# Performance work log

Hardware: AMD Instinct MI355X
Metric: run time of the kernel (lower is better)

Reference implementation:

```python
import jax, jax.numpy as jnp
import numpy as np
import math

BETA = 0.25      # CONFIG['vq_commitment_beta']
DECAY = 0.99     # CONFIG['vq_decay']
EPS = 1e-5

N, D, K = 262144, 64, 512


def setup_inputs() -> dict:
    key = jax.random.key(0)
    k1, k2, k3, k4 = jax.random.split(key, 4)
    z_real = jax.random.normal(k1, (N, D), jnp.float32)
    z_imag = jax.random.normal(k2, (N, D), jnp.float32)
    # embedding init: uniform(-1/K, 1/K); ema_w initialized as a clone
    emb_w = jax.random.uniform(k3, (K, 2 * D), jnp.float32, -1.0 / K, 1.0 / K)
    ema_cluster_size = jnp.zeros((K,), jnp.float32)
    ema_w = emb_w
    return {
        "z_real": z_real,
        "z_imag": z_imag,
        "emb_w": emb_w,
        "ema_cluster_size": ema_cluster_size,
        "ema_w": ema_w,
    }


def reference(z_real, z_imag, emb_w, ema_cluster_size, ema_w):
    n, d = z_real.shape
    k = emb_w.shape[0]
    z_flat = jnp.concatenate([z_real, z_imag], axis=-1)          # [N, 2D]
    # squared euclidean distances to codebook rows
    x_sq = jnp.sum(z_flat ** 2, axis=1, keepdims=True)           # [N, 1]
    y_sq = jnp.sum(emb_w ** 2, axis=1)                           # [K]
    dist = x_sq + y_sq - 2.0 * (z_flat @ emb_w.T)                # [N, K]
    indices = jnp.argmin(dist, axis=-1)                          # [N] int
    z_q = emb_w[indices]                                         # [N, 2D]

    # training-mode EMA update (one-hot matmuls expressed as segment sums)
    ones = jnp.ones((n,), z_flat.dtype)
    n_total = jax.ops.segment_sum(ones, indices, num_segments=k)        # [K]
    new_cluster = ema_cluster_size * DECAY + (1.0 - DECAY) * n_total
    tot = new_cluster.sum()
    cluster_size = (new_cluster + EPS) / (tot + k * EPS) * tot
    dw = jax.ops.segment_sum(z_flat, indices, num_segments=k)           # [K, 2D]
    new_ema_w = ema_w * DECAY + (1.0 - DECAY) * dw
    new_emb_w = new_ema_w / cluster_size[:, None]

    # commitment loss per sample (z_q detached)
    loss_sample = BETA * jnp.mean((jax.lax.stop_gradient(z_q) - z_flat) ** 2, axis=-1)
    # straight-through estimator
    z_q_st = z_flat + jax.lax.stop_gradient(z_q - z_flat)

    probs = n_total / n
    norm_entropy = -jnp.sum(probs * jnp.log(probs + 1e-10)) / math.log(k)

    zq_real = z_q_st[:, :d]
    zq_imag = z_q_st[:, d:]
    return (zq_real, zq_imag, loss_sample, indices, norm_entropy,
            new_emb_w, new_cluster, new_ema_w)
```

## Files before the change

kernel.cpp:

```cpp
#include <hip/hip_runtime.h>

#define NROWS 262144
#define DD 64
#define D2 128
#define KK 512

#define O_ZQR 0
#define O_ZQI 16777216
#define O_LOSS 33554432
#define O_IDX 33816576
#define O_ENT 34078720
#define O_EMB 34078721
#define O_NCL 34144257
#define O_EMA 34144769

typedef __bf16 bf16x8 __attribute__((ext_vector_type(8)));
typedef float f32x4 __attribute__((ext_vector_type(4)));

__device__ __forceinline__ float comb8(const float r[8]) {
  return __fadd_rn(__fadd_rn(__fadd_rn(r[0], r[1]), __fadd_rn(r[2], r[3])),
                   __fadd_rn(__fadd_rn(r[4], r[5]), __fadd_rn(r[6], r[7])));
}

__device__ __forceinline__ ushort f2bf(float x) {
  union { float f; unsigned u; } a; a.f = x;
  unsigned r = (a.u + 0x7FFFu + ((a.u >> 16) & 1u)) >> 16;
  return (ushort)r;
}

__global__ __launch_bounds__(256) void prep_kernel(const float* __restrict__ emb,
    float* __restrict__ ysq, int* __restrict__ nt, float* __restrict__ dw) {
  int t = blockIdx.x * 256 + threadIdx.x;
  dw[t] = 0.f;
  if (t < KK) {
    nt[t] = 0;
    const float* a = emb + t * D2;
    float r[8];
#pragma unroll
    for (int q = 0; q < 8; ++q) { float v = a[q]; r[q] = __fmul_rn(v, v); }
    for (int m = 1; m < 16; ++m)
#pragma unroll
      for (int q = 0; q < 8; ++q) { float v = a[8 * m + q]; r[q] = __fadd_rn(r[q], __fmul_rn(v, v)); }
    ysq[t] = comb8(r);
  }
}

#define BMR 128
#define DELTA 1e-3f
#define LCAP 2048

__global__ __launch_bounds__(512, 2) void vq_mfma(
    const float* __restrict__ zr, const float* __restrict__ zi,
    const float* __restrict__ emb, const float* __restrict__ ysq,
    float* __restrict__ out_zqr, float* __restrict__ out_zqi,
    float* __restrict__ out_loss, float* __restrict__ out_idx,
    int* __restrict__ nt) {
  __shared__ __align__(16) float zf[BMR * 132];
  __shared__ __align__(16) ushort Ab[BMR * 136];
  __shared__ __align__(16) ushort Bb[128 * 136];
  __shared__ float ysql[KK];
  __shared__ float xsql[BMR];
  __shared__ float rowmin[BMR];
  __shared__ ushort lst[LCAP];
  __shared__ float rD[LCAP];
  __shared__ int cnt;
  __shared__ int idxr[BMR];

  const int tid = threadIdx.x;
  const int rowBase = blockIdx.x * BMR;
  const int wv = tid >> 6;
  const int lane = tid & 63;

#pragma unroll
  for (int r = 0; r < 8; ++r) {
    int fidx = r * 512 + tid;
    int row = fidx >> 5, g = fidx & 31;
    float4 v;
    if (g < 16) v = *(const float4*)(zr + (size_t)(rowBase + row) * DD + g * 4);
    else        v = *(const float4*)(zi + (size_t)(rowBase + row) * DD + (g - 16) * 4);
    *(float4*)&zf[row * 132 + g * 4] = v;
  }
  ysql[tid] = ysq[tid];
  if (tid == 0) cnt = 0;
  __syncthreads();

  if (tid < BMR) {
    const float* zp = zf + tid * 132;
    float r8[8];
#pragma unroll
    for (int q = 0; q < 8; ++q) { float z = zp[q]; r8[q] = __fmul_rn(z, z); }
    for (int m = 1; m < 16; ++m)
#pragma unroll
      for (int q = 0; q < 8; ++q) { float z = zp[8 * m + q]; r8[q] = __fadd_rn(r8[q], __fmul_rn(z, z)); }
    xsql[tid] = comb8(r8);
  }
  for (int l = tid; l < BMR * 32; l += 512) {
    int row = l >> 5, seg = l & 31;
    const float* zp = &zf[row * 132 + seg * 4];
    ushort4 u;
    u.x = f2bf(zp[0]); u.y = f2bf(zp[1]); u.z = f2bf(zp[2]); u.w = f2bf(zp[3]);
    *(ushort4*)&Ab[row * 136 + seg * 4] = u;
  }
  __syncthreads();

  bf16x8 af[4];
#pragma unroll
  for (int t = 0; t < 4; ++t)
    af[t] = *(const bf16x8*)&Ab[(16 * wv + (lane & 15)) * 136 + t * 32 + (lane >> 4) * 8];

  float m4[4] = {3.4e38f, 3.4e38f, 3.4e38f, 3.4e38f};

#pragma unroll 1
  for (int phase = 0; phase < 2; ++phase) {
#pragma unroll 1
    for (int c = 0; c < 4; ++c) {
      __syncthreads();
      for (int l = tid; l < 128 * 32; l += 512) {
        int code = l >> 5, seg = l & 31;
        float4 v = *(const float4*)(emb + (size_t)(c * 128 + code) * D2 + seg * 4);
        ushort4 u;
        u.x = f2bf(v.x); u.y = f2bf(v.y); u.z = f2bf(v.z); u.w = f2bf(v.w);
        *(ushort4*)&Bb[code * 136 + seg * 4] = u;
      }
      __syncthreads();

      f32x4 acc[8];
#pragma unroll
      for (int j = 0; j < 8; ++j) acc[j] = (f32x4){0.f, 0.f, 0.f, 0.f};
#pragma unroll
      for (int j = 0; j < 8; ++j)
#pragma unroll
        for (int t = 0; t < 4; ++t) {
          bf16x8 bv = *(const bf16x8*)&Bb[(j * 16 + (lane & 15)) * 136 + t * 32 + (lane >> 4) * 8];
          acc[j] = __builtin_amdgcn_mfma_f32_16x16x32_bf16(af[t], bv, acc[j], 0, 0, 0);
        }

      if (phase == 0) {
#pragma unroll
        for (int j = 0; j < 8; ++j) {
          float y = ysql[c * 128 + j * 16 + (lane & 15)];
#pragma unroll
          for (int r = 0; r < 4; ++r)
            m4[r] = fminf(m4[r], fmaf(-2.f, acc[j][r], y));
        }
      } else {
#pragma unroll
        for (int j = 0; j < 8; ++j) {
          int code = c * 128 + j * 16 + (lane & 15);
          float y = ysql[code];
#pragma unroll
          for (int r = 0; r < 4; ++r) {
            float s = fmaf(-2.f, acc[j][r], y);
            int row = 16 * wv + (lane >> 4) * 4 + r;
            if (s <= rowmin[row] + DELTA) {
              int e = atomicAdd(&cnt, 1);
              if (e < LCAP) lst[e] = (ushort)((row << 9) | code);
            }
          }
        }
      }
    }
    if (phase == 0) {
#pragma unroll
      for (int r = 0; r < 4; ++r) {
        m4[r] = fminf(m4[r], __shfl_xor(m4[r], 1, 64));
        m4[r] = fminf(m4[r], __shfl_xor(m4[r], 2, 64));
        m4[r] = fminf(m4[r], __shfl_xor(m4[r], 4, 64));
        m4[r] = fminf(m4[r], __shfl_xor(m4[r], 8, 64));
      }
      if ((lane & 15) == 0) {
#pragma unroll
        for (int r = 0; r < 4; ++r) rowmin[16 * wv + (lane >> 4) * 4 + r] = m4[r];
      }
      __syncthreads();
    }
  }
  __syncthreads();

  int n = cnt; if (n > LCAP) n = LCAP;
  for (int e = tid; e < n; e += 512) {
    int rc = lst[e];
    int row = rc >> 9, code = rc & 511;
    const float* wrow = emb + (size_t)code * D2;
    const float* zrow = zf + row * 132;
    float a = 0.f;
#pragma unroll 32
    for (int d = 0; d < D2; ++d) a = fmaf(zrow[d], wrow[d], a);
    rD[e] = fmaf(-2.f, a, __fadd_rn(xsql[row], ysql[code]));
  }
  __syncthreads();

  if (tid < BMR) {
    float bD = 3.4e38f; int bc = 1024;
    for (int e = 0; e < n; ++e) {
      int rc = lst[e];
      if ((rc >> 9) == tid) {
        float Dv = rD[e]; int cc = rc & 511;
        if (Dv < bD || (Dv == bD && cc < bc)) { bD = Dv; bc = cc; }
      }
    }
    idxr[tid] = bc;
    out_idx[rowBase + tid] = (float)bc;
    atomicAdd(&nt[bc], 1);
  }
  __syncthreads();

  {
    int m = tid & 15, rsub = tid >> 4;
#pragma unroll
    for (int p = 0; p < 8; ++p) {
      int half = p & 1;
      int row = (p >> 1) * 32 + rsub;
      int bi = idxr[row];
      float4 e4 = *(const float4*)(emb + (size_t)bi * D2 + half * DD + m * 4);
      float4 z4 = *(const float4*)&zf[row * 132 + half * DD + m * 4];
      float4 o;
      o.x = __fadd_rn(z4.x, __fsub_rn(e4.x, z4.x));
      o.y = __fadd_rn(z4.y, __fsub_rn(e4.y, z4.y));
      o.z = __fadd_rn(z4.z, __fsub_rn(e4.z, z4.z));
      o.w = __fadd_rn(z4.w, __fsub_rn(e4.w, z4.w));
      float* outp = half ? (out_zqi + (size_t)(rowBase + row) * DD + m * 4)
                         : (out_zqr + (size_t)(rowBase + row) * DD + m * 4);
      *(float4*)outp = o;
    }
  }

  if (tid < BMR) {
    int bi = idxr[tid];
    const float* erow = emb + (size_t)bi * D2;
    const float* zp = zf + tid * 132;
    float r8[8];
#pragma unroll
    for (int q = 0; q < 8; ++q) {
      float df = __fsub_rn(erow[q], zp[q]);
      r8[q] = __fmul_rn(df, df);
    }
    for (int m = 1; m < 16; ++m)
#pragma unroll
      for (int q = 0; q < 8; ++q) {
        float df = __fsub_rn(erow[8 * m + q], zp[8 * m + q]);
        r8[q] = __fadd_rn(r8[q], __fmul_rn(df, df));
      }
    float S = comb8(r8);
    out_loss[rowBase + tid] = __fmul_rn(0.25f, S / 128.0f);
  }
}

__global__ __launch_bounds__(256) void dw_scatter(const float* __restrict__ zr,
    const float* __restrict__ zi, const float* __restrict__ idxf,
    float* __restrict__ dw) {
  __shared__ float tab[KK * 32];
  int tid = threadIdx.x;
  int dc = blockIdx.x & 3;
  int rb = blockIdx.x >> 2;
  for (int l = tid; l < KK * 32; l += 256) tab[l] = 0.f;
  __syncthreads();
  int r = tid >> 5, c = tid & 31;
  const float* zsrc = (dc < 2) ? zr : zi;
  int colBase = (dc & 1) * 32;
  int rowBase = rb * 1024;
  int row = rowBase + r;
  int idx = (int)idxf[row];
  float v = zsrc[(size_t)row * DD + colBase + c];
  for (int it = 0; it < 127; ++it) {
    int nrow = rowBase + (it + 1) * 8 + r;
    int nidx = (int)idxf[nrow];
    float nv = zsrc[(size_t)nrow * DD + colBase + c];
    atomicAdd(&tab[idx * 32 + c], v);
    idx = nidx; v = nv;
  }
  atomicAdd(&tab[idx * 32 + c], v);
  __syncthreads();
  for (int l = tid; l < KK * 32; l += 256) {
    int k = l >> 5, cc = l & 31;
    atomicAdd(&dw[k * D2 + dc * 32 + cc], tab[l]);
  }
}

__device__ float pw128(const float* a) {
  float r[8];
#pragma unroll
  for (int q = 0; q < 8; ++q) r[q] = a[q];
  for (int m = 1; m < 16; ++m)
#pragma unroll
    for (int q = 0; q < 8; ++q) r[q] = __fadd_rn(r[q], a[8 * m + q]);
  return comb8(r);
}

__global__ __launch_bounds__(512) void finalize_kernel(const int* __restrict__ nt,
    const float* __restrict__ ema_cs, float* __restrict__ out_ncl,
    float* __restrict__ out_ent, float* __restrict__ csize) {
  __shared__ float arr[KK];
  __shared__ float term[KK];
  __shared__ float tot_s;
  int t = threadIdx.x;
  float c = (float)nt[t];
  float newc = __fadd_rn(__fmul_rn(ema_cs[t], 0.99f), __fmul_rn(0.01f, c));
  out_ncl[t] = newc;
  arr[t] = newc;
  float p = c / 262144.f;
  term[t] = __fmul_rn(p, logf(__fadd_rn(p, 1e-10f)));
  __syncthreads();
  if (t == 0) {
    float tot = __fadd_rn(__fadd_rn(pw128(arr), pw128(arr + 128)),
                          __fadd_rn(pw128(arr + 256), pw128(arr + 384)));
    tot_s = tot;
    float S = __fadd_rn(__fadd_rn(pw128(term), pw128(term + 128)),
                        __fadd_rn(pw128(term + 256), pw128(term + 384)));
    out_ent[0] = __fdiv_rn(-S, 6.2383246250395075f);
  }
  __syncthreads();
  float tot = tot_s;
  float cs = __fmul_rn(__fdiv_rn(__fadd_rn(arr[t], 1e-5f), __fadd_rn(tot, 0.00512f)), tot);
  csize[t] = cs;
}

__global__ __launch_bounds__(256) void ema_out_kernel(const float* __restrict__ ema_w,
    const float* __restrict__ dw, const float* __restrict__ csize,
    float* __restrict__ out_ema, float* __restrict__ out_emb) {
  int t = blockIdx.x * 256 + threadIdx.x;
  float e = __fadd_rn(__fmul_rn(ema_w[t], 0.99f), __fmul_rn(0.01f, dw[t]));
  out_ema[t] = e;
  out_emb[t] = __fdiv_rn(e, csize[t >> 7]);
}

extern "C" void kernel_launch(void* const* d_in, const int* in_sizes, int n_in,
                              void* d_out, int out_size, void* d_ws, size_t ws_size,
                              hipStream_t stream) {
  const float* zr     = (const float*)d_in[0];
  const float* zi     = (const float*)d_in[1];
  const float* emb    = (const float*)d_in[2];
  const float* ema_cs = (const float*)d_in[3];
  const float* ema_w  = (const float*)d_in[4];
  float* out = (float*)d_out;

  float* wsf   = (float*)d_ws;
  float* ysq   = wsf;
  float* csize = wsf + 512;
  int*   nt    = (int*)(wsf + 1024);
  float* dw    = wsf + 1536;

  prep_kernel<<<256, 256, 0, stream>>>(emb, ysq, nt, dw);
  vq_mfma<<<NROWS / BMR, 512, 0, stream>>>(zr, zi, emb, ysq,
      out + O_ZQR, out + O_ZQI, out + O_LOSS, out + O_IDX, nt);
  dw_scatter<<<1024, 256, 0, stream>>>(zr, zi, out + O_IDX, dw);
  finalize_kernel<<<1, 512, 0, stream>>>(nt, ema_cs, out + O_NCL, out + O_ENT, csize);
  ema_out_kernel<<<256, 256, 0, stream>>>(ema_w, dw, csize, out + O_EMA, out + O_EMB);
}
```

Measured before the change: 796.0 us.

## Precompute bf16 codebook, double-buffer codebook tiles, and use packed atomicMin argmin

The prep kernel now converts the codebook to bf16 once, so the main kernel no longer reconverts it in every block. Codebook tiles are double-buffered in LDS with a register prefetch of the next tile, which cuts barriers per chunk and overlaps global loads with MFMA work. A fragments are converted straight from the fp32 tile, which removes the Ab staging buffer. The per-row serial scan over the candidate list is replaced by a 64-bit packed (distance, code) atomicMin in LDS. That ordering is only correct for non-negative distances, and the exact re-check now reads z from global memory instead of LDS.

```diff
diff --git a/kernel.cpp b/kernel.cpp
--- a/kernel.cpp
+++ b/kernel.cpp
@@ -29,9 +29,11 @@
 }
 
 __global__ __launch_bounds__(256) void prep_kernel(const float* __restrict__ emb,
-    float* __restrict__ ysq, int* __restrict__ nt, float* __restrict__ dw) {
+    float* __restrict__ ysq, int* __restrict__ nt, float* __restrict__ dw,
+    ushort* __restrict__ embbf) {
   int t = blockIdx.x * 256 + threadIdx.x;
   dw[t] = 0.f;
+  embbf[t] = f2bf(emb[t]);
   if (t < KK) {
     nt[t] = 0;
     const float* a = emb + t * D2;
@@ -48,21 +50,22 @@
 #define BMR 128
 #define DELTA 1e-3f
 #define LCAP 2048
+#define BST 136
 
 __global__ __launch_bounds__(512, 2) void vq_mfma(
     const float* __restrict__ zr, const float* __restrict__ zi,
-    const float* __restrict__ emb, const float* __restrict__ ysq,
+    const float* __restrict__ emb, const ushort* __restrict__ embbf,
+    const float* __restrict__ ysq,
     float* __restrict__ out_zqr, float* __restrict__ out_zqi,
     float* __restrict__ out_loss, float* __restrict__ out_idx,
     int* __restrict__ nt) {
   __shared__ __align__(16) float zf[BMR * 132];
-  __shared__ __align__(16) ushort Ab[BMR * 136];
-  __shared__ __align__(16) ushort Bb[128 * 136];
+  __shared__ __align__(16) ushort Bb[2][128 * BST];
   __shared__ float ysql[KK];
   __shared__ float xsql[BMR];
   __shared__ float rowmin[BMR];
+  __shared__ unsigned long long rowbest[BMR];
   __shared__ ushort lst[LCAP];
-  __shared__ float rD[LCAP];
   __shared__ int cnt;
   __shared__ int idxr[BMR];
 
@@ -80,7 +83,15 @@
     else        v = *(const float4*)(zi + (size_t)(rowBase + row) * DD + (g - 16) * 4);
     *(float4*)&zf[row * 132 + g * 4] = v;
   }
+#pragma unroll
+  for (int it = 0; it < 4; ++it) {
+    int gidx = it * 512 + tid;
+    int row = gidx >> 4, slot = gidx & 15;
+    *(uint4*)&Bb[0][row * BST + slot * 8] =
+        *(const uint4*)(embbf + (size_t)row * D2 + slot * 8);
+  }
   ysql[tid] = ysq[tid];
+  if (tid < BMR) rowbest[tid] = ~0ull;
   if (tid == 0) cnt = 0;
   __syncthreads();
 
@@ -94,111 +105,116 @@
       for (int q = 0; q < 8; ++q) { float z = zp[8 * m + q]; r8[q] = __fadd_rn(r8[q], __fmul_rn(z, z)); }
     xsql[tid] = comb8(r8);
   }
-  for (int l = tid; l < BMR * 32; l += 512) {
-    int row = l >> 5, seg = l & 31;
-    const float* zp = &zf[row * 132 + seg * 4];
-    ushort4 u;
-    u.x = f2bf(zp[0]); u.y = f2bf(zp[1]); u.z = f2bf(zp[2]); u.w = f2bf(zp[3]);
-    *(ushort4*)&Ab[row * 136 + seg * 4] = u;
-  }
-  __syncthreads();
 
   bf16x8 af[4];
-#pragma unroll
-  for (int t = 0; t < 4; ++t)
-    af[t] = *(const bf16x8*)&Ab[(16 * wv + (lane & 15)) * 136 + t * 32 + (lane >> 4) * 8];
+  {
+    int arow = 16 * wv + (lane & 15);
+#pragma unroll
+    for (int t4 = 0; t4 < 4; ++t4) {
+      union { ushort u[8]; bf16x8 v; } a;
+#pragma unroll
+      for (int e = 0; e < 8; ++e)
+        a.u[e] = f2bf(zf[arow * 132 + t4 * 32 + (lane >> 4) * 8 + e]);
+      af[t4] = a.v;
+    }
+  }
 
   float m4[4] = {3.4e38f, 3.4e38f, 3.4e38f, 3.4e38f};
 
 #pragma unroll 1
-  for (int phase = 0; phase < 2; ++phase) {
-#pragma unroll 1
-    for (int c = 0; c < 4; ++c) {
-      __syncthreads();
-      for (int l = tid; l < 128 * 32; l += 512) {
-        int code = l >> 5, seg = l & 31;
-        float4 v = *(const float4*)(emb + (size_t)(c * 128 + code) * D2 + seg * 4);
-        ushort4 u;
-        u.x = f2bf(v.x); u.y = f2bf(v.y); u.z = f2bf(v.z); u.w = f2bf(v.w);
-        *(ushort4*)&Bb[code * 136 + seg * 4] = u;
-      }
-      __syncthreads();
-
-      f32x4 acc[8];
-#pragma unroll
-      for (int j = 0; j < 8; ++j) acc[j] = (f32x4){0.f, 0.f, 0.f, 0.f};
-#pragma unroll
-      for (int j = 0; j < 8; ++j)
-#pragma unroll
-        for (int t = 0; t < 4; ++t) {
-          bf16x8 bv = *(const bf16x8*)&Bb[(j * 16 + (lane & 15)) * 136 + t * 32 + (lane >> 4) * 8];
-          acc[j] = __builtin_amdgcn_mfma_f32_16x16x32_bf16(af[t], bv, acc[j], 0, 0, 0);
+  for (int p = 0; p < 8; ++p) {
+    const int cNext = (p + 1) & 3;
+    uint4 stg0, stg1, stg2, stg3;
+    if (p < 7) {
+      int row0 = tid >> 3, seg = tid & 7;
+      const uint4* src = (const uint4*)(embbf + (size_t)cNext * 128 * D2);
+      stg0 = src[(size_t)row0 * 16 + seg];
+      stg1 = src[(size_t)(row0 + 64) * 16 + seg];
+      stg2 = src[(size_t)row0 * 16 + seg + 8];
+      stg3 = src[(size_t)(row0 + 64) * 16 + seg + 8];
+    }
+    const ushort* Bp = &Bb[p & 1][0];
+    f32x4 acc[8];
+#pragma unroll
+    for (int j = 0; j < 8; ++j) acc[j] = (f32x4){0.f, 0.f, 0.f, 0.f};
+#pragma unroll
+    for (int j = 0; j < 8; ++j)
+#pragma unroll
+      for (int t4 = 0; t4 < 4; ++t4) {
+        bf16x8 bv = *(const bf16x8*)&Bp[(j * 16 + (lane & 15)) * BST + t4 * 32 + (lane >> 4) * 8];
+        acc[j] = __builtin_amdgcn_mfma_f32_16x16x32_bf16(af[t4], bv, acc[j], 0, 0, 0);
+      }
+
+    if (p < 4) {
+#pragma unroll
+      for (int j = 0; j < 8; ++j) {
+        float y = ysql[(p & 3) * 128 + j * 16 + (lane & 15)];
+#pragma unroll
+        for (int r = 0; r < 4; ++r)
+          m4[r] = fminf(m4[r], fmaf(-2.f, acc[j][r], y));
+      }
+      if (p == 3) {
+#pragma unroll
+        for (int r = 0; r < 4; ++r) {
+          m4[r] = fminf(m4[r], __shfl_xor(m4[r], 1, 64));
+          m4[r] = fminf(m4[r], __shfl_xor(m4[r], 2, 64));
+          m4[r] = fminf(m4[r], __shfl_xor(m4[r], 4, 64));
+          m4[r] = fminf(m4[r], __shfl_xor(m4[r], 8, 64));
         }
-
-      if (phase == 0) {
-#pragma unroll
-        for (int j = 0; j < 8; ++j) {
-          float y = ysql[c * 128 + j * 16 + (lane & 15)];
-#pragma unroll
-          for (int r = 0; r < 4; ++r)
-            m4[r] = fminf(m4[r], fmaf(-2.f, acc[j][r], y));
+        if ((lane & 15) == 0) {
+#pragma unroll
+          for (int r = 0; r < 4; ++r) rowmin[16 * wv + (lane >> 4) * 4 + r] = m4[r];
         }
-      } else {
-#pragma unroll
-        for (int j = 0; j < 8; ++j) {
-          int code = c * 128 + j * 16 + (lane & 15);
-          float y = ysql[code];
-#pragma unroll
-          for (int r = 0; r < 4; ++r) {
-            float s = fmaf(-2.f, acc[j][r], y);
-            int row = 16 * wv + (lane >> 4) * 4 + r;
-            if (s <= rowmin[row] + DELTA) {
-              int e = atomicAdd(&cnt, 1);
-              if (e < LCAP) lst[e] = (ushort)((row << 9) | code);
-            }
+      }
+    } else {
+#pragma unroll
+      for (int j = 0; j < 8; ++j) {
+        int code = (p & 3) * 128 + j * 16 + (lane & 15);
+        float y = ysql[code];
+#pragma unroll
+        for (int r = 0; r < 4; ++r) {
+          float s = fmaf(-2.f, acc[j][r], y);
+          int row = 16 * wv + (lane >> 4) * 4 + r;
+          if (s <= rowmin[row] + DELTA) {
+            int e = atomicAdd(&cnt, 1);
+            if (e < LCAP) lst[e] = (ushort)((row << 9) | code);
           }
         }
       }
     }
-    if (phase == 0) {
-#pragma unroll
-      for (int r = 0; r < 4; ++r) {
-        m4[r] = fminf(m4[r], __shfl_xor(m4[r], 1, 64));
-        m4[r] = fminf(m4[r], __shfl_xor(m4[r], 2, 64));
-        m4[r] = fminf(m4[r], __shfl_xor(m4[r], 4, 64));
-        m4[r] = fminf(m4[r], __shfl_xor(m4[r], 8, 64));
-      }
-      if ((lane & 15) == 0) {
-#pragma unroll
-        for (int r = 0; r < 4; ++r) rowmin[16 * wv + (lane >> 4) * 4 + r] = m4[r];
-      }
-      __syncthreads();
-    }
-  }
-  __syncthreads();
+
+    if (p < 7) {
+      ushort* Bw = &Bb[(p + 1) & 1][0];
+      int row0 = tid >> 3, seg = tid & 7;
+      *(uint4*)&Bw[(size_t)row0 * BST + seg * 8] = stg0;
+      *(uint4*)&Bw[(size_t)(row0 + 64) * BST + seg * 8] = stg1;
+      *(uint4*)&Bw[(size_t)row0 * BST + (seg + 8) * 8] = stg2;
+      *(uint4*)&Bw[(size_t)(row0 + 64) * BST + (seg + 8) * 8] = stg3;
+    }
+    __syncthreads();
+  }
 
   int n = cnt; if (n > LCAP) n = LCAP;
   for (int e = tid; e < n; e += 512) {
     int rc = lst[e];
     int row = rc >> 9, code = rc & 511;
     const float* wrow = emb + (size_t)code * D2;
-    const float* zrow = zf + row * 132;
+    const float* zrr = zr + (size_t)(rowBase + row) * DD;
+    const float* zii = zi + (size_t)(rowBase + row) * DD;
     float a = 0.f;
-#pragma unroll 32
-    for (int d = 0; d < D2; ++d) a = fmaf(zrow[d], wrow[d], a);
-    rD[e] = fmaf(-2.f, a, __fadd_rn(xsql[row], ysql[code]));
+#pragma unroll 16
+    for (int d = 0; d < DD; ++d) a = fmaf(zrr[d], wrow[d], a);
+#pragma unroll 16
+    for (int d = 0; d < DD; ++d) a = fmaf(zii[d], wrow[DD + d], a);
+    float Dv = fmaf(-2.f, a, __fadd_rn(xsql[row], ysql[code]));
+    unsigned long long pack =
+        ((unsigned long long)__float_as_uint(Dv) << 32) | (unsigned)code;
+    atomicMin(&rowbest[row], pack);
   }
   __syncthreads();
 
   if (tid < BMR) {
-    float bD = 3.4e38f; int bc = 1024;
-    for (int e = 0; e < n; ++e) {
-      int rc = lst[e];
-      if ((rc >> 9) == tid) {
-        float Dv = rD[e]; int cc = rc & 511;
-        if (Dv < bD || (Dv == bD && cc < bc)) { bD = Dv; bc = cc; }
-      }
-    }
+    int bc = (int)(rowbest[tid] & 0xFFFFFFFFull);
     idxr[tid] = bc;
     out_idx[rowBase + tid] = (float)bc;
     atomicAdd(&nt[bc], 1);
@@ -339,9 +355,10 @@
   float* csize = wsf + 512;
   int*   nt    = (int*)(wsf + 1024);
   float* dw    = wsf + 1536;
-
-  prep_kernel<<<256, 256, 0, stream>>>(emb, ysq, nt, dw);
-  vq_mfma<<<NROWS / BMR, 512, 0, stream>>>(zr, zi, emb, ysq,
+  ushort* embbf = (ushort*)(wsf + 67072);
+
+  prep_kernel<<<256, 256, 0, stream>>>(emb, ysq, nt, dw, embbf);
+  vq_mfma<<<NROWS / BMR, 512, 0, stream>>>(zr, zi, emb, embbf, ysq,
       out + O_ZQR, out + O_ZQI, out + O_LOSS, out + O_IDX, nt);
   dw_scatter<<<1024, 256, 0, stream>>>(zr, zi, out + O_IDX, dw);
   finalize_kernel<<<1, 512, 0, stream>>>(nt, ema_cs, out + O_NCL, out + O_ENT, csize);
```

Measured after the change: 638.1 us. -19.8%, faster.
